# Kernel optimization log

Hardware: AMD Instinct MI355X
Metric: run time of the kernel (lower is better)

## Reference

```python
import jax, jax.numpy as jnp
import numpy as np

N_NODES = 50000
N_EDGES = 800000
IN_DIM, H1, H2, OUT_DIM = 128, 117, 42, 24


def _glorot(key, fan_in, fan_out):
    lim = (6.0 / (fan_in + fan_out)) ** 0.5
    return jax.random.uniform(key, (fan_in, fan_out), jnp.float32, -lim, lim)


def setup_inputs() -> dict:
    key = jax.random.key(0)
    ks = jax.random.split(key, 16)
    x = jax.random.normal(ks[0], (N_NODES, IN_DIM), jnp.float32)
    edge_index = jax.random.randint(ks[1], (2, N_EDGES), 0, N_NODES, dtype=jnp.int64)
    dims = [(IN_DIM, H1), (H1, H2), (H2, OUT_DIM), (H2, OUT_DIM)]
    names = ["1", "2", "mu", "lv"]
    inp = {"x": x, "edge_index": edge_index}
    for i, ((di, do), nm) in enumerate(zip(dims, names)):
        inp[f"Wl_{nm}"] = _glorot(ks[2 + 3 * i], di, do)      # weight on aggregated neighbors
        inp[f"Wr_{nm}"] = _glorot(ks[3 + 3 * i], di, do)      # root (self) weight
        inp[f"b_{nm}"] = jnp.zeros((do,), jnp.float32)
    return inp


def _sage_conv(x, src, dst, Wl, Wr, b):
    # mean-aggregate source features onto target nodes (PyG SAGEConv, aggr='mean')
    agg = jax.ops.segment_sum(x[src], dst, num_segments=N_NODES)      # [N, d_in]
    deg = jax.ops.segment_sum(jnp.ones((src.shape[0], 1), x.dtype), dst,
                              num_segments=N_NODES)                    # [N, 1]
    agg = agg / jnp.maximum(deg, 1.0)
    return agg @ Wl + x @ Wr + b


def reference(x, edge_index, Wl_1, Wr_1, b_1, Wl_2, Wr_2, b_2,
              Wl_mu, Wr_mu, b_mu, Wl_lv, Wr_lv, b_lv):
    src, dst = edge_index[0], edge_index[1]
    h = jax.nn.relu(_sage_conv(x, src, dst, Wl_1, Wr_1, b_1))          # dropout = identity (eval)
    h = jax.nn.relu(_sage_conv(h, src, dst, Wl_2, Wr_2, b_2))
    mu = _sage_conv(h, src, dst, Wl_mu, Wr_mu, b_mu)
    logvar = _sage_conv(h, src, dst, Wl_lv, Wr_lv, b_lv)
    return (mu, logvar)
```

## Files before the change

### kernel.cpp

```cpp
#include <hip/hip_runtime.h>

#define N_NODES 50000
#define N_EDGES 800000
#define CAP 64
#define ZROW 50000

typedef _Float16 f16;
typedef unsigned short u16;
typedef f16 f16x2 __attribute__((ext_vector_type(2)));
typedef f16 f16x4 __attribute__((ext_vector_type(4)));
typedef f16 f16x8 __attribute__((ext_vector_type(8)));
typedef float f32x4 __attribute__((ext_vector_type(4)));

#if __has_builtin(__builtin_amdgcn_fdot2)
#define FDOT2(a, b, c) __builtin_amdgcn_fdot2((a), (b), (c), false)
#else
#define FDOT2(a, b, c) ((c) + (float)(a).x * (float)(b).x + (float)(a).y * (float)(b).y)
#endif

__global__ void k_fill(u16* __restrict__ bucket, int* __restrict__ cnt,
                       f16* __restrict__ t1l, f16* __restrict__ t2l,
                       f16* __restrict__ p) {
    int gt = blockIdx.x * 256 + threadIdx.x;
    if (gt < 400000) {
        uint4 pat = {0xC350C350u, 0xC350C350u, 0xC350C350u, 0xC350C350u};
        ((uint4*)bucket)[gt] = pat;
    }
    if (gt < N_NODES) cnt[gt] = 0;
    if (blockIdx.x == 1599) {
        int t = threadIdx.x;
        if (t < 64)       ((unsigned*)t1l)[(size_t)ZROW * 64 + t] = 0u;
        else if (t < 96)  ((unsigned*)t2l)[(size_t)ZROW * 32 + (t - 64)] = 0u;
        else if (t < 128) ((unsigned*)p)[(size_t)ZROW * 32 + (t - 96)] = 0u;
    }
}

__global__ void k_build(const int* __restrict__ ei, int* __restrict__ cnt,
                        u16* __restrict__ bucket) {
    int e = blockIdx.x * blockDim.x + threadIdx.x;
    if (e >= N_EDGES) return;
    int s = ei[e];
    int d = ei[N_EDGES + e];
    int pos = atomicAdd(&cnt[d], 1);
    if (pos < CAP) bucket[d * CAP + pos] = (u16)s;
}

__global__ void k_packw(const float* __restrict__ Wl1, const float* __restrict__ Wr1,
                        const float* __restrict__ Wl2, const float* __restrict__ Wr2,
                        const float* __restrict__ Wlm, const float* __restrict__ Wrm,
                        const float* __restrict__ Wlv, const float* __restrict__ Wrv,
                        f16x2* __restrict__ w2p, f16* __restrict__ w1b,
                        f16* __restrict__ w2b) {
    int t = blockIdx.x * blockDim.x + threadIdx.x;
    if (t < 42 * 48) {
        int k = t / 48, j = t % 48;
        int o = (j < 24) ? j : j - 24;
        const float* L = (j < 24) ? Wlm : Wlv;
        const float* R = (j < 24) ? Wrm : Wrv;
        f16x2 w; w.x = (f16)L[k * 24 + o]; w.y = (f16)R[k * 24 + o];
        w2p[t] = w;
    }
    if (t < 15 * 4 * 64 * 8) {
        int f = t >> 9;
        int r = t & 511;
        int lane = r >> 3, j = r & 7;
        int nt = f >> 2, s = f & 3;
        int k = s * 32 + (lane >> 4) * 8 + j;
        int col = nt * 16 + (lane & 15);
        float v = 0.f;
        if (col < 117) v = Wl1[k * 117 + col];
        else if (col < 234) v = Wr1[k * 117 + (col - 117)];
        w1b[t] = (f16)v;
    }
    if (t < 6 * 4 * 64 * 8) {
        int f = t >> 9;
        int r = t & 511;
        int lane = r >> 3, j = r & 7;
        int nt = f >> 2, s = f & 3;
        int k = s * 32 + (lane >> 4) * 8 + j;
        int col = nt * 16 + (lane & 15);
        float v = 0.f;
        if (k < 117) {
            if (col < 42)      v = Wl2[k * 42 + col];
            else if (col < 84) v = Wr2[k * 42 + (col - 42)];
        }
        w2b[t] = (f16)v;
    }
}

__global__ __launch_bounds__(256) void k_gemm1(const float* __restrict__ x,
                        const f16* __restrict__ w1b, const float* __restrict__ b1,
                        f16* __restrict__ t1l, float* __restrict__ t1r) {
    int base = blockIdx.x * 16;
    int t = threadIdx.x;
    __shared__ __align__(16) f16 xa[16 * 128];
    {
        int row = t >> 4, kc = t & 15;
        const float4* xp = (const float4*)(x + (size_t)(base + row) * 128 + kc * 8);
        float4 x0 = xp[0], x1 = xp[1];
        f16x8 hv;
        hv[0] = (f16)x0.x; hv[1] = (f16)x0.y; hv[2] = (f16)x0.z; hv[3] = (f16)x0.w;
        hv[4] = (f16)x1.x; hv[5] = (f16)x1.y; hv[6] = (f16)x1.z; hv[7] = (f16)x1.w;
        int byte = row * 256 + ((kc ^ (row & 7)) << 4);
        *(f16x8*)((char*)xa + byte) = hv;
    }
    __syncthreads();
    int lane = t & 63, w = t >> 6;
    int hi = lane >> 4, lo = lane & 15;
    f16x8 a[4];
#pragma unroll
    for (int s = 0; s < 4; ++s) {
        int kchunk = s * 4 + hi;
        int byte = lo * 256 + ((kchunk ^ (lo & 7)) << 4);
        a[s] = *(const f16x8*)((const char*)xa + byte);
    }
    int ntiles = (w < 3) ? 4 : 3;
    for (int i = 0; i < ntiles; ++i) {
        int nt = w * 4 + i;
        const f16x8* bp = (const f16x8*)w1b + (size_t)(nt * 4) * 64 + lane;
        f32x4 acc = {0.f, 0.f, 0.f, 0.f};
#pragma unroll
        for (int s = 0; s < 4; ++s)
            acc = __builtin_amdgcn_mfma_f32_16x16x32_f16(a[s], bp[s * 64], acc, 0, 0, 0);
        int gcol = nt * 16 + lo;
#pragma unroll
        for (int r = 0; r < 4; ++r) {
            int grow = base + hi * 4 + r;
            float val = acc[r];
            if (gcol < 117) {
                t1l[(size_t)grow * 128 + gcol] = (f16)val;
            } else if (nt == 7) {
                t1l[(size_t)grow * 128 + gcol] = (f16)0.f;
            }
            if (gcol >= 117) {
                int c2 = gcol - 117;
                if (c2 < 117)      t1r[(size_t)grow * 120 + c2] = val + b1[c2];
                else if (c2 < 120) t1r[(size_t)grow * 120 + c2] = 0.f;
            }
        }
    }
}

__global__ __launch_bounds__(512) void k_fused1(
        const f16* __restrict__ t1l, const float* __restrict__ t1r,
        const int* __restrict__ cnt, const u16* __restrict__ bucket,
        const f16* __restrict__ w2b, const float* __restrict__ b2,
        f16* __restrict__ t2l, float* __restrict__ s2) {
    __shared__ __align__(16) f16 h1[16 * 128];
    int t = threadIdx.x;
    int lane = t & 63, w = t >> 6;
    int tilebase = blockIdx.x * 16;
    int iA = tilebase + w * 2, iB = iA + 1;
    int cA = cnt[iA], cB = cnt[iB];
    int nA = cA > CAP ? CAP : cA, nB = cB > CAP ? CAP : cB;
    int idsA = (int)bucket[(size_t)iA * CAP + lane];
    int idsB = (int)bucket[(size_t)iB * CAP + lane];
    int g = (lane < 30) ? 0 : 1;
    int d = lane - 30 * g;
    bool act = (lane < 60);
    int i_my = g ? iB : iA;
    float deg = fmaxf((float)(g ? cB : cA), 1.f);
    int dd = d < 31 ? d : 31;
    int nmax = nA > nB ? nA : nB;
    float ax = 0.f, ay = 0.f, az = 0.f, aw = 0.f;
    const char* base = (const char*)t1l;
    const f16x2 e10 = {(f16)1.f, (f16)0.f};
    const f16x2 e01 = {(f16)0.f, (f16)1.f};
    for (int e0 = 0; e0 < nmax; e0 += 16) {
        f16x4 v[16];
#pragma unroll
        for (int u = 0; u < 16; ++u) {
            int e = (e0 + u) & 63;
            int ra = __builtin_amdgcn_readlane(idsA, e);
            int rb = __builtin_amdgcn_readlane(idsB, e);
            int id = g ? rb : ra;
            unsigned off = ((unsigned)id << 8) + ((unsigned)dd << 3);
            v[u] = *(const f16x4*)(base + off);
        }
#pragma unroll
        for (int u = 0; u < 16; ++u) {
            f16x2 lo = __builtin_shufflevector(v[u], v[u], 0, 1);
            f16x2 hi2 = __builtin_shufflevector(v[u], v[u], 2, 3);
            ax = FDOT2(lo, e10, ax);
            ay = FDOT2(lo, e01, ay);
            az = FDOT2(hi2, e10, az);
            aw = FDOT2(hi2, e01, aw);
        }
    }
    int trow = w * 2 + g;
    if (act) {
        float4 s = ((const float4*)(t1r + (size_t)i_my * 120))[d];
        f16x4 hv;
        hv.x = (f16)fmaxf(ax / deg + s.x, 0.f);
        hv.y = (f16)fmaxf(ay / deg + s.y, 0.f);
        hv.z = (f16)fmaxf(az / deg + s.z, 0.f);
        hv.w = (f16)fmaxf(aw / deg + s.w, 0.f);
        int chunk = d >> 1;
        int byte = trow * 256 + ((chunk ^ (trow & 7)) << 4) + ((d & 1) << 3);
        *(f16x4*)((char*)h1 + byte) = hv;
    } else {
        int r2 = w * 2 + ((lane - 60) >> 1);
        int byte = r2 * 256 + ((15 ^ (r2 & 7)) << 4) + ((lane & 1) << 3);
        f16x4 z = {(f16)0.f, (f16)0.f, (f16)0.f, (f16)0.f};
        *(f16x4*)((char*)h1 + byte) = z;
    }
    __syncthreads();
    if (w < 6) {
        int lo = lane & 15, hi = lane >> 4;
        f16x8 a[4];
#pragma unroll
        for (int s = 0; s < 4; ++s) {
            int kc = s * 4 + hi;
            int byte = lo * 256 + ((kc ^ (lo & 7)) << 4);
            a[s] = *(const f16x8*)((const char*)h1 + byte);
        }
        const f16x8* bp = (const f16x8*)w2b + (size_t)(w * 4) * 64 + lane;
        f32x4 acc = {0.f, 0.f, 0.f, 0.f};
#pragma unroll
        for (int s = 0; s < 4; ++s)
            acc = __builtin_amdgcn_mfma_f32_16x16x32_f16(a[s], bp[s * 64], acc, 0, 0, 0);
        int col = w * 16 + lo;
        if (col < 42) {
#pragma unroll
            for (int r = 0; r < 4; ++r) {
                int node = tilebase + hi * 4 + r;
                t2l[(size_t)node * 64 + col] = (f16)acc[r];
            }
        } else if (col < 84) {
            int c2 = col - 42;
            float bb = b2[c2];
#pragma unroll
            for (int r = 0; r < 4; ++r) {
                int node = tilebase + hi * 4 + r;
                s2[(size_t)node * 42 + c2] = acc[r] + bb;
            }
        }
    }
}

__global__ __launch_bounds__(128) void k_fused2(
        const f16* __restrict__ t2l, const float* __restrict__ s2,
        const int* __restrict__ cnt, const u16* __restrict__ bucket,
        const f16x2* __restrict__ w2p,
        const float* __restrict__ bm, const float* __restrict__ bv,
        f16* __restrict__ p, float* __restrict__ out) {
    __shared__ __align__(16) float h2[2][3][48];
    int t = threadIdx.x;
    int lane = t & 63, wv = t >> 6;
    int i0 = blockIdx.x * 6 + wv * 3;
    int iA = i0, iB = i0 + 1, iC = i0 + 2;
    bool vA = iA < N_NODES, vB = iB < N_NODES, vC = iC < N_NODES;
    int cA = vA ? cnt[iA] : 0, cB = vB ? cnt[iB] : 0, cC = vC ? cnt[iC] : 0;
    int nA = cA > CAP ? CAP : cA, nB = cB > CAP ? CAP : cB, nC = cC > CAP ? CAP : cC;
    int idsA = vA ? (int)bucket[(size_t)iA * CAP + lane] : ZROW;
    int idsB = vB ? (int)bucket[(size_t)iB * CAP + lane] : ZROW;
    int idsC = vC ? (int)bucket[(size_t)iC * CAP + lane] : ZROW;
    int g = (lane < 21) ? 0 : (lane < 42 ? 1 : 2);
    int d = lane - 21 * g;
    bool act = (lane < 63);
    int i_my = i0 + g;
    bool valid = act && (i_my < N_NODES);
    float deg = fmaxf((float)(g == 0 ? cA : (g == 1 ? cB : cC)), 1.f);
    int nmax = nA > nB ? nA : nB; if (nC > nmax) nmax = nC;
    float ax = 0.f, ay = 0.f;
    const char* base = (const char*)t2l;
    const f16x2 e10 = {(f16)1.f, (f16)0.f};
    const f16x2 e01 = {(f16)0.f, (f16)1.f};
    for (int e0 = 0; e0 < nmax; e0 += 16) {
        f16x2 v[16];
#pragma unroll
        for (int u = 0; u < 16; ++u) {
            int e = (e0 + u) & 63;
            int ra = __builtin_amdgcn_readlane(idsA, e);
            int rb = __builtin_amdgcn_readlane(idsB, e);
            int rc = __builtin_amdgcn_readlane(idsC, e);
            int id = (g == 0) ? ra : ((g == 1) ? rb : rc);
            unsigned off = ((unsigned)id << 7) + ((unsigned)d << 2);
            v[u] = *(const f16x2*)(base + off);
        }
#pragma unroll
        for (int u = 0; u < 16; ++u) {
            ax = FDOT2(v[u], e10, ax);
            ay = FDOT2(v[u], e01, ay);
        }
    }
    if (valid && d < 21) {
        float2 s = ((const float2*)(s2 + (size_t)i_my * 42))[d];
        h2[wv][g][2 * d]     = fmaxf(ax / deg + s.x, 0.f);
        h2[wv][g][2 * d + 1] = fmaxf(ay / deg + s.y, 0.f);
    }
    __syncthreads();
    int j = lane;
    if (j < 48) {
        int o = (j < 24) ? j : j - 24;
        float bias = (j < 24) ? bm[o] : bv[o];
        float pA = 0.f, pB = 0.f, pC = 0.f, qA = 0.f, qB = 0.f, qC = 0.f;
        const float4* hA = (const float4*)&h2[wv][0][0];
        const float4* hB = (const float4*)&h2[wv][1][0];
        const float4* hC = (const float4*)&h2[wv][2][0];
#pragma unroll 2
        for (int kk = 0; kk < 10; ++kk) {
            float4 a = hA[kk], b = hB[kk], c = hC[kk];
            float av[4] = {a.x, a.y, a.z, a.w};
            float bv4[4] = {b.x, b.y, b.z, b.w};
            float cv[4] = {c.x, c.y, c.z, c.w};
#pragma unroll
            for (int u = 0; u < 4; ++u) {
                int k = 4 * kk + u;
                f16x2 wvv = w2p[k * 48 + j];
                float wl = (float)wvv.x, wr = (float)wvv.y;
                pA = fmaf(av[u], wl, pA);  qA = fmaf(av[u], wr, qA);
                pB = fmaf(bv4[u], wl, pB); qB = fmaf(bv4[u], wr, qB);
                pC = fmaf(cv[u], wl, pC);  qC = fmaf(cv[u], wr, qC);
            }
        }
        for (int k = 40; k < 42; ++k) {
            f16x2 wvv = w2p[k * 48 + j];
            float wl = (float)wvv.x, wr = (float)wvv.y;
            pA = fmaf(h2[wv][0][k], wl, pA); qA = fmaf(h2[wv][0][k], wr, qA);
            pB = fmaf(h2[wv][1][k], wl, pB); qB = fmaf(h2[wv][1][k], wr, qB);
            pC = fmaf(h2[wv][2][k], wl, pC); qC = fmaf(h2[wv][2][k], wr, qC);
        }
        size_t half = (j < 24) ? 0 : (size_t)N_NODES * 24;
        if (vA) { p[(size_t)iA * 64 + j] = (f16)pA; out[half + (size_t)iA * 24 + o] = qA + bias; }
        if (vB) { p[(size_t)iB * 64 + j] = (f16)pB; out[half + (size_t)iB * 24 + o] = qB + bias; }
        if (vC) { p[(size_t)iC * 64 + j] = (f16)pC; out[half + (size_t)iC * 24 + o] = qC + bias; }
    }
}

__global__ __launch_bounds__(128) void k_final(
        const f16* __restrict__ p, const int* __restrict__ cnt,
        const u16* __restrict__ bucket, float* __restrict__ out) {
    int t = threadIdx.x;
    int lane = t & 63, wv = t >> 6;
    int iA = blockIdx.x * 4 + wv * 2, iB = iA + 1;
    int cA = cnt[iA], cB = cnt[iB];
    int nA = cA > CAP ? CAP : cA, nB = cB > CAP ? CAP : cB;
    int idsA = (int)bucket[(size_t)iA * CAP + lane];
    int idsB = (int)bucket[(size_t)iB * CAP + lane];
    int g = (lane < 24) ? 0 : 1;
    int d = lane - 24 * g;
    bool act = (lane < 48);
    int i_my = g ? iB : iA;
    float deg = fmaxf((float)(g ? cB : cA), 1.f);
    int dd = d < 31 ? d : 31;
    int nmax = nA > nB ? nA : nB;
    float ax = 0.f, ay = 0.f;
    const char* base = (const char*)p;
    const f16x2 e10 = {(f16)1.f, (f16)0.f};
    const f16x2 e01 = {(f16)0.f, (f16)1.f};
    for (int e0 = 0; e0 < nmax; e0 += 16) {
        f16x2 v[16];
#pragma unroll
        for (int u = 0; u < 16; ++u) {
            int e = (e0 + u) & 63;
            int ra = __builtin_amdgcn_readlane(idsA, e);
            int rb = __builtin_amdgcn_readlane(idsB, e);
            int id = g ? rb : ra;
            unsigned off = ((unsigned)id << 7) + ((unsigned)dd << 2);
            v[u] = *(const f16x2*)(base + off);
        }
#pragma unroll
        for (int u = 0; u < 16; ++u) {
            ax = FDOT2(v[u], e10, ax);
            ay = FDOT2(v[u], e01, ay);
        }
    }
    if (act) {
        float mx = ax / deg, my = ay / deg;
        size_t addr = (d < 12) ? ((size_t)i_my * 24 + 2 * d)
                               : ((size_t)N_NODES * 24 + (size_t)i_my * 24 + 2 * (d - 12));
        float2 s = *(const float2*)(out + addr);
        float2 r; r.x = s.x + mx; r.y = s.y + my;
        *(float2*)(out + addr) = r;
    }
}

extern "C" void kernel_launch(void* const* d_in, const int* in_sizes, int n_in,
                              void* d_out, int out_size, void* d_ws, size_t ws_size,
                              hipStream_t stream) {
    const float* x   = (const float*)d_in[0];
    const int*   ei  = (const int*)d_in[1];
    const float* Wl1 = (const float*)d_in[2];
    const float* Wr1 = (const float*)d_in[3];
    const float* b1  = (const float*)d_in[4];
    const float* Wl2 = (const float*)d_in[5];
    const float* Wr2 = (const float*)d_in[6];
    const float* b2  = (const float*)d_in[7];
    const float* Wlm = (const float*)d_in[8];
    const float* Wrm = (const float*)d_in[9];
    const float* bm  = (const float*)d_in[10];
    const float* Wlv = (const float*)d_in[11];
    const float* Wrv = (const float*)d_in[12];
    const float* bv  = (const float*)d_in[13];
    float* out = (float*)d_out;

    char* ws = (char*)d_ws;
    int*   cnt    = (int*)(ws);
    u16*   bucket = (u16*)(ws + 204800);
    f16*   t1l    = (f16*)(ws + 6604800);
    float* t1r    = (float*)(ws + 19405312);
    f16*   t2l    = (f16*)(ws + 43405312);
    float* s2     = (float*)(ws + 49805824);
    f16*   w1b    = (f16*)(ws + 49805824);
    f16*   p      = (f16*)(ws + 58205824);
    f16x2* w2p    = (f16x2*)(ws + 64606208);
    f16*   w2b    = (f16*)(ws + 64614400);

    k_fill<<<1600, 256, 0, stream>>>(bucket, cnt, t1l, t2l, p);
    k_packw<<<120, 256, 0, stream>>>(Wl1, Wr1, Wl2, Wr2, Wlm, Wrm, Wlv, Wrv,
                                     w2p, w1b, w2b);
    k_build<<<(N_EDGES + 255) / 256, 256, 0, stream>>>(ei, cnt, bucket);
    k_gemm1<<<N_NODES / 16, 256, 0, stream>>>(x, w1b, b1, t1l, t1r);
    k_fused1<<<N_NODES / 16, 512, 0, stream>>>(t1l, t1r, cnt, bucket, w2b, b2, t2l, s2);
    k_fused2<<<(N_NODES + 5) / 6, 128, 0, stream>>>(t2l, s2, cnt, bucket,
                                                    w2p, bm, bv, p, out);
    k_final<<<N_NODES / 4, 128, 0, stream>>>(p, cnt, bucket, out);
}
```

Baseline: 247.5 us.

## Merge setup kernels, stage neighbor ids in LDS, use 16-byte gathers and MFMA heads

After: 209.4 us. -15.4%, faster.

```diff
diff --git a/kernel.cpp b/kernel.cpp
--- a/kernel.cpp
+++ b/kernel.cpp
@@ -18,9 +18,15 @@
 #define FDOT2(a, b, c) ((c) + (float)(a).x * (float)(b).x + (float)(a).y * (float)(b).y)
 #endif
 
-__global__ void k_fill(u16* __restrict__ bucket, int* __restrict__ cnt,
-                       f16* __restrict__ t1l, f16* __restrict__ t2l,
-                       f16* __restrict__ p) {
+__global__ void k_fillpack(u16* __restrict__ bucket, int* __restrict__ cnt,
+                           f16* __restrict__ t1l, f16* __restrict__ t2l,
+                           f16* __restrict__ p,
+                           const float* __restrict__ Wl1, const float* __restrict__ Wr1,
+                           const float* __restrict__ Wl2, const float* __restrict__ Wr2,
+                           const float* __restrict__ Wlm, const float* __restrict__ Wrm,
+                           const float* __restrict__ Wlv, const float* __restrict__ Wrv,
+                           f16* __restrict__ w1b, f16* __restrict__ w2b,
+                           f16* __restrict__ w3b) {
     int gt = blockIdx.x * 256 + threadIdx.x;
     if (gt < 400000) {
         uint4 pat = {0xC350C350u, 0xC350C350u, 0xC350C350u, 0xC350C350u};
@@ -33,36 +39,8 @@
         else if (t < 96)  ((unsigned*)t2l)[(size_t)ZROW * 32 + (t - 64)] = 0u;
         else if (t < 128) ((unsigned*)p)[(size_t)ZROW * 32 + (t - 96)] = 0u;
     }
-}
-
-__global__ void k_build(const int* __restrict__ ei, int* __restrict__ cnt,
-                        u16* __restrict__ bucket) {
-    int e = blockIdx.x * blockDim.x + threadIdx.x;
-    if (e >= N_EDGES) return;
-    int s = ei[e];
-    int d = ei[N_EDGES + e];
-    int pos = atomicAdd(&cnt[d], 1);
-    if (pos < CAP) bucket[d * CAP + pos] = (u16)s;
-}
-
-__global__ void k_packw(const float* __restrict__ Wl1, const float* __restrict__ Wr1,
-                        const float* __restrict__ Wl2, const float* __restrict__ Wr2,
-                        const float* __restrict__ Wlm, const float* __restrict__ Wrm,
-                        const float* __restrict__ Wlv, const float* __restrict__ Wrv,
-                        f16x2* __restrict__ w2p, f16* __restrict__ w1b,
-                        f16* __restrict__ w2b) {
-    int t = blockIdx.x * blockDim.x + threadIdx.x;
-    if (t < 42 * 48) {
-        int k = t / 48, j = t % 48;
-        int o = (j < 24) ? j : j - 24;
-        const float* L = (j < 24) ? Wlm : Wlv;
-        const float* R = (j < 24) ? Wrm : Wrv;
-        f16x2 w; w.x = (f16)L[k * 24 + o]; w.y = (f16)R[k * 24 + o];
-        w2p[t] = w;
-    }
-    if (t < 15 * 4 * 64 * 8) {
-        int f = t >> 9;
-        int r = t & 511;
+    if (gt < 15 * 4 * 64 * 8) {
+        int f = gt >> 9, r = gt & 511;
         int lane = r >> 3, j = r & 7;
         int nt = f >> 2, s = f & 3;
         int k = s * 32 + (lane >> 4) * 8 + j;
@@ -70,29 +48,50 @@
         float v = 0.f;
         if (col < 117) v = Wl1[k * 117 + col];
         else if (col < 234) v = Wr1[k * 117 + (col - 117)];
-        w1b[t] = (f16)v;
-    }
-    if (t < 6 * 4 * 64 * 8) {
-        int f = t >> 9;
-        int r = t & 511;
+        w1b[gt] = (f16)v;
+    }
+    if (gt < 6 * 4 * 64 * 8) {
+        int f = gt >> 9, r = gt & 511;
         int lane = r >> 3, j = r & 7;
         int nt = f >> 2, s = f & 3;
         int k = s * 32 + (lane >> 4) * 8 + j;
         int col = nt * 16 + (lane & 15);
         float v = 0.f;
         if (k < 117) {
-            if (col < 42)      v = Wl2[k * 42 + col];
-            else if (col < 84) v = Wr2[k * 42 + (col - 42)];
-        }
-        w2b[t] = (f16)v;
-    }
-}
-
-__global__ __launch_bounds__(256) void k_gemm1(const float* __restrict__ x,
+            if (col < 42)                     v = Wl2[k * 42 + col];
+            else if (col >= 48 && col < 90)   v = Wr2[k * 42 + (col - 48)];
+        }
+        w2b[gt] = (f16)v;
+    }
+    if (gt < 6 * 2 * 64 * 8) {
+        int f = gt >> 9, r = gt & 511;
+        int lane = r >> 3, j = r & 7;
+        int ct = f >> 1, s = f & 1;
+        int k = s * 32 + (lane >> 4) * 8 + j;
+        int col = ct * 16 + (lane & 15);
+        float v = 0.f;
+        if (k < 42) {
+            if (col < 24)      v = Wlm[k * 24 + col];
+            else if (col < 48) v = Wlv[k * 24 + (col - 24)];
+            else if (col < 72) v = Wrm[k * 24 + (col - 48)];
+            else               v = Wrv[k * 24 + (col - 72)];
+        }
+        w3b[gt] = (f16)v;
+    }
+}
+
+__global__ __launch_bounds__(256) void k_bg(const int* __restrict__ ei,
+                        int* __restrict__ cnt, u16* __restrict__ bucket,
+                        const float* __restrict__ x,
                         const f16* __restrict__ w1b, const float* __restrict__ b1,
                         f16* __restrict__ t1l, float* __restrict__ t1r) {
+    int t = threadIdx.x;
+    int e = blockIdx.x * 256 + t;
+    int se = ei[e];
+    int de = ei[N_EDGES + e];
+    int pos = atomicAdd(&cnt[de], 1);
+
     int base = blockIdx.x * 16;
-    int t = threadIdx.x;
     __shared__ __align__(16) f16 xa[16 * 128];
     {
         int row = t >> 4, kc = t & 15;
@@ -139,6 +138,7 @@
             }
         }
     }
+    if (pos < CAP) bucket[de * CAP + pos] = (u16)se;
 }
 
 __global__ __launch_bounds__(512) void k_fused1(
@@ -146,93 +146,89 @@
         const int* __restrict__ cnt, const u16* __restrict__ bucket,
         const f16* __restrict__ w2b, const float* __restrict__ b2,
         f16* __restrict__ t2l, float* __restrict__ s2) {
-    __shared__ __align__(16) f16 h1[16 * 128];
+    __shared__ __align__(16) f16 h1[32 * 128];
+    __shared__ __align__(16) u16 ids[32 * 72];
     int t = threadIdx.x;
     int lane = t & 63, w = t >> 6;
-    int tilebase = blockIdx.x * 16;
-    int iA = tilebase + w * 2, iB = iA + 1;
-    int cA = cnt[iA], cB = cnt[iB];
-    int nA = cA > CAP ? CAP : cA, nB = cB > CAP ? CAP : cB;
-    int idsA = (int)bucket[(size_t)iA * CAP + lane];
-    int idsB = (int)bucket[(size_t)iB * CAP + lane];
-    int g = (lane < 30) ? 0 : 1;
-    int d = lane - 30 * g;
-    bool act = (lane < 60);
-    int i_my = g ? iB : iA;
-    float deg = fmaxf((float)(g ? cB : cA), 1.f);
-    int dd = d < 31 ? d : 31;
-    int nmax = nA > nB ? nA : nB;
-    float ax = 0.f, ay = 0.f, az = 0.f, aw = 0.f;
-    const char* base = (const char*)t1l;
+    int tilebase = blockIdx.x * 32;
+    if (t < 256) {
+        uint4 q = ((const uint4*)(bucket + (size_t)tilebase * CAP))[t];
+        int nl = t >> 3, c = t & 7;
+        *(uint4*)(ids + nl * 72 + c * 8) = q;
+    }
+    int g = (lane < 60) ? (lane / 15) : 3;
+    int d = (lane < 60) ? (lane - g * 15) : 14;
+    int nl = w * 4 + g;
+    int i_my = tilebase + nl;
+    int c = (i_my < N_NODES && lane < 60) ? cnt[i_my] : 0;
+    int n = min(c, CAP);
+    float deg = fmaxf((float)c, 1.f);
+    int n0 = __builtin_amdgcn_readlane(n, 0),  n1 = __builtin_amdgcn_readlane(n, 15);
+    int n2 = __builtin_amdgcn_readlane(n, 30), n3 = __builtin_amdgcn_readlane(n, 45);
+    int nmax = max(max(n0, n1), max(n2, n3));
+    __syncthreads();
+    float acc[8] = {0.f, 0.f, 0.f, 0.f, 0.f, 0.f, 0.f, 0.f};
+    const char* tb = (const char*)t1l;
+    unsigned doff = (unsigned)d * 16;
     const f16x2 e10 = {(f16)1.f, (f16)0.f};
     const f16x2 e01 = {(f16)0.f, (f16)1.f};
-    for (int e0 = 0; e0 < nmax; e0 += 16) {
-        f16x4 v[16];
-#pragma unroll
-        for (int u = 0; u < 16; ++u) {
-            int e = (e0 + u) & 63;
-            int ra = __builtin_amdgcn_readlane(idsA, e);
-            int rb = __builtin_amdgcn_readlane(idsB, e);
-            int id = g ? rb : ra;
-            unsigned off = ((unsigned)id << 8) + ((unsigned)dd << 3);
-            v[u] = *(const f16x4*)(base + off);
-        }
-#pragma unroll
-        for (int u = 0; u < 16; ++u) {
-            f16x2 lo = __builtin_shufflevector(v[u], v[u], 0, 1);
-            f16x2 hi2 = __builtin_shufflevector(v[u], v[u], 2, 3);
-            ax = FDOT2(lo, e10, ax);
-            ay = FDOT2(lo, e01, ay);
-            az = FDOT2(hi2, e10, az);
-            aw = FDOT2(hi2, e01, aw);
-        }
-    }
-    int trow = w * 2 + g;
-    if (act) {
-        float4 s = ((const float4*)(t1r + (size_t)i_my * 120))[d];
-        f16x4 hv;
-        hv.x = (f16)fmaxf(ax / deg + s.x, 0.f);
-        hv.y = (f16)fmaxf(ay / deg + s.y, 0.f);
-        hv.z = (f16)fmaxf(az / deg + s.z, 0.f);
-        hv.w = (f16)fmaxf(aw / deg + s.w, 0.f);
-        int chunk = d >> 1;
-        int byte = trow * 256 + ((chunk ^ (trow & 7)) << 4) + ((d & 1) << 3);
-        *(f16x4*)((char*)h1 + byte) = hv;
+    int idb = nl * 72;
+    for (int e0 = 0; e0 < nmax; e0 += 8) {
+        f16x8 v[8];
+#pragma unroll
+        for (int u = 0; u < 8; ++u) {
+            unsigned id = ids[idb + e0 + u];
+            v[u] = *(const f16x8*)(tb + id * 256u + doff);
+        }
+#pragma unroll
+        for (int u = 0; u < 8; ++u) {
+            const f16x2* pv = (const f16x2*)&v[u];
+#pragma unroll
+            for (int j = 0; j < 4; ++j) {
+                acc[2 * j]     = FDOT2(pv[j], e10, acc[2 * j]);
+                acc[2 * j + 1] = FDOT2(pv[j], e01, acc[2 * j + 1]);
+            }
+        }
+    }
+    if (lane < 60) {
+        int i_ld = (i_my < N_NODES) ? i_my : 0;
+        const float4* sp = (const float4*)(t1r + (size_t)i_ld * 120 + 8 * d);
+        float4 s0 = sp[0], s1 = sp[1];
+        float sv[8] = {s0.x, s0.y, s0.z, s0.w, s1.x, s1.y, s1.z, s1.w};
+        f16x8 hv;
+#pragma unroll
+        for (int j = 0; j < 8; ++j) hv[j] = (f16)fmaxf(acc[j] / deg + sv[j], 0.f);
+        int byte = nl * 256 + ((d ^ (nl & 7)) << 4);
+        *(f16x8*)((char*)h1 + byte) = hv;
     } else {
-        int r2 = w * 2 + ((lane - 60) >> 1);
-        int byte = r2 * 256 + ((15 ^ (r2 & 7)) << 4) + ((lane & 1) << 3);
-        f16x4 z = {(f16)0.f, (f16)0.f, (f16)0.f, (f16)0.f};
-        *(f16x4*)((char*)h1 + byte) = z;
-    }
-    __syncthreads();
-    if (w < 6) {
-        int lo = lane & 15, hi = lane >> 4;
+        int row = w * 4 + (lane - 60);
+        int byte = row * 256 + ((15 ^ (row & 7)) << 4);
+        f16x8 z = {};
+        *(f16x8*)((char*)h1 + byte) = z;
+    }
+    __syncthreads();
+    int lo = lane & 15, hi = lane >> 4;
+    for (int jj = w; jj < 12; jj += 8) {
+        int ct = jj >> 1, rh = jj & 1;
+        int row = rh * 16 + lo;
         f16x8 a[4];
 #pragma unroll
         for (int s = 0; s < 4; ++s) {
             int kc = s * 4 + hi;
-            int byte = lo * 256 + ((kc ^ (lo & 7)) << 4);
-            a[s] = *(const f16x8*)((const char*)h1 + byte);
-        }
-        const f16x8* bp = (const f16x8*)w2b + (size_t)(w * 4) * 64 + lane;
-        f32x4 acc = {0.f, 0.f, 0.f, 0.f};
+            a[s] = *(const f16x8*)((const char*)h1 + row * 256 + ((kc ^ (row & 7)) << 4));
+        }
+        const f16x8* bp = (const f16x8*)w2b + (size_t)(ct * 4) * 64 + lane;
+        f32x4 acc4 = {0.f, 0.f, 0.f, 0.f};
 #pragma unroll
         for (int s = 0; s < 4; ++s)
-            acc = __builtin_amdgcn_mfma_f32_16x16x32_f16(a[s], bp[s * 64], acc, 0, 0, 0);
-        int col = w * 16 + lo;
-        if (col < 42) {
-#pragma unroll
-            for (int r = 0; r < 4; ++r) {
-                int node = tilebase + hi * 4 + r;
-                t2l[(size_t)node * 64 + col] = (f16)acc[r];
-            }
-        } else if (col < 84) {
-            int c2 = col - 42;
-            float bb = b2[c2];
-#pragma unroll
-            for (int r = 0; r < 4; ++r) {
-                int node = tilebase + hi * 4 + r;
-                s2[(size_t)node * 42 + c2] = acc[r] + bb;
+            acc4 = __builtin_amdgcn_mfma_f32_16x16x32_f16(a[s], bp[s * 64], acc4, 0, 0, 0);
+        int col = ct * 16 + lo;
+#pragma unroll
+        for (int r = 0; r < 4; ++r) {
+            int node = tilebase + rh * 16 + hi * 4 + r;
+            if (node < N_NODES) {
+                if (col < 48)      t2l[(size_t)node * 64 + col] = (f16)acc4[r];
+                else if (col < 90) s2[(size_t)node * 42 + (col - 48)] = acc4[r] + b2[col - 48];
             }
         }
     }
@@ -241,138 +237,166 @@
 __global__ __launch_bounds__(128) void k_fused2(
         const f16* __restrict__ t2l, const float* __restrict__ s2,
         const int* __restrict__ cnt, const u16* __restrict__ bucket,
-        const f16x2* __restrict__ w2p,
+        const f16* __restrict__ w3b,
         const float* __restrict__ bm, const float* __restrict__ bv,
         f16* __restrict__ p, float* __restrict__ out) {
-    __shared__ __align__(16) float h2[2][3][48];
+    __shared__ __align__(16) f16 h2[16 * 64];
+    __shared__ __align__(16) u16 ids[16 * 72];
     int t = threadIdx.x;
     int lane = t & 63, wv = t >> 6;
-    int i0 = blockIdx.x * 6 + wv * 3;
-    int iA = i0, iB = i0 + 1, iC = i0 + 2;
-    bool vA = iA < N_NODES, vB = iB < N_NODES, vC = iC < N_NODES;
-    int cA = vA ? cnt[iA] : 0, cB = vB ? cnt[iB] : 0, cC = vC ? cnt[iC] : 0;
-    int nA = cA > CAP ? CAP : cA, nB = cB > CAP ? CAP : cB, nC = cC > CAP ? CAP : cC;
-    int idsA = vA ? (int)bucket[(size_t)iA * CAP + lane] : ZROW;
-    int idsB = vB ? (int)bucket[(size_t)iB * CAP + lane] : ZROW;
-    int idsC = vC ? (int)bucket[(size_t)iC * CAP + lane] : ZROW;
-    int g = (lane < 21) ? 0 : (lane < 42 ? 1 : 2);
-    int d = lane - 21 * g;
-    bool act = (lane < 63);
-    int i_my = i0 + g;
-    bool valid = act && (i_my < N_NODES);
-    float deg = fmaxf((float)(g == 0 ? cA : (g == 1 ? cB : cC)), 1.f);
-    int nmax = nA > nB ? nA : nB; if (nC > nmax) nmax = nC;
-    float ax = 0.f, ay = 0.f;
-    const char* base = (const char*)t2l;
+    int nb = blockIdx.x * 16;
+    {
+        uint4 q = ((const uint4*)(bucket + (size_t)nb * CAP))[t];
+        int nl = t >> 3, c = t & 7;
+        *(uint4*)(ids + nl * 72 + c * 8) = q;
+    }
+    int g = (lane < 48) ? (lane / 6) : 7;
+    int d = (lane < 48) ? (lane - g * 6) : 5;
+    int nl = wv * 8 + g;
+    int i_my = nb + nl;
+    int c = (lane < 48) ? cnt[i_my] : 0;
+    int n = min(c, CAP);
+    float deg = fmaxf((float)c, 1.f);
+    int nmax = n;
+#pragma unroll
+    for (int m = 1; m < 64; m <<= 1) nmax = max(nmax, __shfl_xor(nmax, m));
+    __syncthreads();
+    float acc[8] = {0.f, 0.f, 0.f, 0.f, 0.f, 0.f, 0.f, 0.f};
+    const char* tb = (const char*)t2l;
+    unsigned doff = (unsigned)d * 16;
     const f16x2 e10 = {(f16)1.f, (f16)0.f};
     const f16x2 e01 = {(f16)0.f, (f16)1.f};
-    for (int e0 = 0; e0 < nmax; e0 += 16) {
-        f16x2 v[16];
-#pragma unroll
-        for (int u = 0; u < 16; ++u) {
-            int e = (e0 + u) & 63;
-            int ra = __builtin_amdgcn_readlane(idsA, e);
-            int rb = __builtin_amdgcn_readlane(idsB, e);
-            int rc = __builtin_amdgcn_readlane(idsC, e);
-            int id = (g == 0) ? ra : ((g == 1) ? rb : rc);
-            unsigned off = ((unsigned)id << 7) + ((unsigned)d << 2);
-            v[u] = *(const f16x2*)(base + off);
-        }
-#pragma unroll
-        for (int u = 0; u < 16; ++u) {
-            ax = FDOT2(v[u], e10, ax);
-            ay = FDOT2(v[u], e01, ay);
-        }
-    }
-    if (valid && d < 21) {
-        float2 s = ((const float2*)(s2 + (size_t)i_my * 42))[d];
-        h2[wv][g][2 * d]     = fmaxf(ax / deg + s.x, 0.f);
-        h2[wv][g][2 * d + 1] = fmaxf(ay / deg + s.y, 0.f);
-    }
-    __syncthreads();
-    int j = lane;
-    if (j < 48) {
-        int o = (j < 24) ? j : j - 24;
-        float bias = (j < 24) ? bm[o] : bv[o];
-        float pA = 0.f, pB = 0.f, pC = 0.f, qA = 0.f, qB = 0.f, qC = 0.f;
-        const float4* hA = (const float4*)&h2[wv][0][0];
-        const float4* hB = (const float4*)&h2[wv][1][0];
-        const float4* hC = (const float4*)&h2[wv][2][0];
-#pragma unroll 2
-        for (int kk = 0; kk < 10; ++kk) {
-            float4 a = hA[kk], b = hB[kk], c = hC[kk];
-            float av[4] = {a.x, a.y, a.z, a.w};
-            float bv4[4] = {b.x, b.y, b.z, b.w};
-            float cv[4] = {c.x, c.y, c.z, c.w};
-#pragma unroll
-            for (int u = 0; u < 4; ++u) {
-                int k = 4 * kk + u;
-                f16x2 wvv = w2p[k * 48 + j];
-                float wl = (float)wvv.x, wr = (float)wvv.y;
-                pA = fmaf(av[u], wl, pA);  qA = fmaf(av[u], wr, qA);
-                pB = fmaf(bv4[u], wl, pB); qB = fmaf(bv4[u], wr, qB);
-                pC = fmaf(cv[u], wl, pC);  qC = fmaf(cv[u], wr, qC);
-            }
-        }
-        for (int k = 40; k < 42; ++k) {
-            f16x2 wvv = w2p[k * 48 + j];
-            float wl = (float)wvv.x, wr = (float)wvv.y;
-            pA = fmaf(h2[wv][0][k], wl, pA); qA = fmaf(h2[wv][0][k], wr, qA);
-            pB = fmaf(h2[wv][1][k], wl, pB); qB = fmaf(h2[wv][1][k], wr, qB);
-            pC = fmaf(h2[wv][2][k], wl, pC); qC = fmaf(h2[wv][2][k], wr, qC);
-        }
-        size_t half = (j < 24) ? 0 : (size_t)N_NODES * 24;
-        if (vA) { p[(size_t)iA * 64 + j] = (f16)pA; out[half + (size_t)iA * 24 + o] = qA + bias; }
-        if (vB) { p[(size_t)iB * 64 + j] = (f16)pB; out[half + (size_t)iB * 24 + o] = qB + bias; }
-        if (vC) { p[(size_t)iC * 64 + j] = (f16)pC; out[half + (size_t)iC * 24 + o] = qC + bias; }
+    int idb = nl * 72;
+    for (int e0 = 0; e0 < nmax; e0 += 8) {
+        f16x8 v[8];
+#pragma unroll
+        for (int u = 0; u < 8; ++u) {
+            unsigned id = ids[idb + e0 + u];
+            v[u] = *(const f16x8*)(tb + id * 128u + doff);
+        }
+#pragma unroll
+        for (int u = 0; u < 8; ++u) {
+            const f16x2* pv = (const f16x2*)&v[u];
+#pragma unroll
+            for (int j = 0; j < 4; ++j) {
+                acc[2 * j]     = FDOT2(pv[j], e10, acc[2 * j]);
+                acc[2 * j + 1] = FDOT2(pv[j], e01, acc[2 * j + 1]);
+            }
+        }
+    }
+    if (lane < 48) {
+        float sv[8];
+        if (d < 5) {
+            const float4* sp = (const float4*)(s2 + (size_t)i_my * 42 + 8 * d);
+            float4 s0 = sp[0], s1 = sp[1];
+            sv[0] = s0.x; sv[1] = s0.y; sv[2] = s0.z; sv[3] = s0.w;
+            sv[4] = s1.x; sv[5] = s1.y; sv[6] = s1.z; sv[7] = s1.w;
+        } else {
+            float2 s0 = *(const float2*)(s2 + (size_t)i_my * 42 + 40);
+            sv[0] = s0.x; sv[1] = s0.y;
+            sv[2] = sv[3] = sv[4] = sv[5] = sv[6] = sv[7] = 0.f;
+        }
+        f16x8 hv;
+#pragma unroll
+        for (int j = 0; j < 8; ++j) hv[j] = (f16)fmaxf(acc[j] / deg + sv[j], 0.f);
+        int byte = nl * 128 + ((d ^ (nl & 7)) << 4);
+        *(f16x8*)((char*)h2 + byte) = hv;
+    } else {
+        int j = lane - 48;
+        int row = wv * 8 + (j >> 1);
+        int chunk = 6 + (j & 1);
+        int byte = row * 128 + ((chunk ^ (row & 7)) << 4);
+        f16x8 z = {};
+        *(f16x8*)((char*)h2 + byte) = z;
+    }
+    __syncthreads();
+    int lo = lane & 15, hi = lane >> 4;
+    f16x8 a2[2];
+#pragma unroll
+    for (int s = 0; s < 2; ++s) {
+        int kc = s * 4 + hi;
+        a2[s] = *(const f16x8*)((const char*)h2 + lo * 128 + ((kc ^ (lo & 7)) << 4));
+    }
+#pragma unroll
+    for (int i = 0; i < 3; ++i) {
+        int ct = wv * 3 + i;
+        const f16x8* bp = (const f16x8*)w3b + (size_t)(ct * 2) * 64 + lane;
+        f32x4 acc4 = {0.f, 0.f, 0.f, 0.f};
+        acc4 = __builtin_amdgcn_mfma_f32_16x16x32_f16(a2[0], bp[0], acc4, 0, 0, 0);
+        acc4 = __builtin_amdgcn_mfma_f32_16x16x32_f16(a2[1], bp[64], acc4, 0, 0, 0);
+        int col = ct * 16 + lo;
+#pragma unroll
+        for (int r = 0; r < 4; ++r) {
+            int node = nb + hi * 4 + r;
+            if (col < 48) {
+                p[(size_t)node * 64 + col] = (f16)acc4[r];
+            } else {
+                int o = col - 48;
+                if (o < 24) out[(size_t)node * 24 + o] = acc4[r] + bm[o];
+                else out[(size_t)N_NODES * 24 + (size_t)node * 24 + (o - 24)] = acc4[r] + bv[o - 24];
+            }
+        }
     }
 }
 
 __global__ __launch_bounds__(128) void k_final(
         const f16* __restrict__ p, const int* __restrict__ cnt,
         const u16* __restrict__ bucket, float* __restrict__ out) {
+    __shared__ __align__(16) u16 ids[20 * 72];
     int t = threadIdx.x;
     int lane = t & 63, wv = t >> 6;
-    int iA = blockIdx.x * 4 + wv * 2, iB = iA + 1;
-    int cA = cnt[iA], cB = cnt[iB];
-    int nA = cA > CAP ? CAP : cA, nB = cB > CAP ? CAP : cB;
-    int idsA = (int)bucket[(size_t)iA * CAP + lane];
-    int idsB = (int)bucket[(size_t)iB * CAP + lane];
-    int g = (lane < 24) ? 0 : 1;
-    int d = lane - 24 * g;
-    bool act = (lane < 48);
-    int i_my = g ? iB : iA;
-    float deg = fmaxf((float)(g ? cB : cA), 1.f);
-    int dd = d < 31 ? d : 31;
-    int nmax = nA > nB ? nA : nB;
-    float ax = 0.f, ay = 0.f;
-    const char* base = (const char*)p;
+    int nb = blockIdx.x * 20;
+    for (int s = t; s < 160; s += 128) {
+        uint4 q = ((const uint4*)(bucket + (size_t)nb * CAP))[s];
+        int nl = s >> 3, c = s & 7;
+        *(uint4*)(ids + nl * 72 + c * 8) = q;
+    }
+    int g = (lane < 60) ? (lane / 6) : 9;
+    int d = (lane < 60) ? (lane - g * 6) : 5;
+    int nl = wv * 10 + g;
+    int i_my = nb + nl;
+    int c = (lane < 60) ? cnt[i_my] : 0;
+    int n = min(c, CAP);
+    float deg = fmaxf((float)c, 1.f);
+    int nmax = n;
+#pragma unroll
+    for (int m = 1; m < 64; m <<= 1) nmax = max(nmax, __shfl_xor(nmax, m));
+    __syncthreads();
+    float acc[8] = {0.f, 0.f, 0.f, 0.f, 0.f, 0.f, 0.f, 0.f};
+    const char* pb = (const char*)p;
+    unsigned doff = (unsigned)d * 16;
     const f16x2 e10 = {(f16)1.f, (f16)0.f};
     const f16x2 e01 = {(f16)0.f, (f16)1.f};
-    for (int e0 = 0; e0 < nmax; e0 += 16) {
-        f16x2 v[16];
-#pragma unroll
-        for (int u = 0; u < 16; ++u) {
-            int e = (e0 + u) & 63;
-            int ra = __builtin_amdgcn_readlane(idsA, e);
-            int rb = __builtin_amdgcn_readlane(idsB, e);
-            int id = g ? rb : ra;
-            unsigned off = ((unsigned)id << 7) + ((unsigned)dd << 2);
-            v[u] = *(const f16x2*)(base + off);
-        }
-#pragma unroll
-        for (int u = 0; u < 16; ++u) {
-            ax = FDOT2(v[u], e10, ax);
-            ay = FDOT2(v[u], e01, ay);
-        }
-    }
-    if (act) {
-        float mx = ax / deg, my = ay / deg;
-        size_t addr = (d < 12) ? ((size_t)i_my * 24 + 2 * d)
-                               : ((size_t)N_NODES * 24 + (size_t)i_my * 24 + 2 * (d - 12));
-        float2 s = *(const float2*)(out + addr);
-        float2 r; r.x = s.x + mx; r.y = s.y + my;
-        *(float2*)(out + addr) = r;
+    int idb = nl * 72;
+    for (int e0 = 0; e0 < nmax; e0 += 8) {
+        f16x8 v[8];
+#pragma unroll
+        for (int u = 0; u < 8; ++u) {
+            unsigned id = ids[idb + e0 + u];
+            v[u] = *(const f16x8*)(pb + id * 128u + doff);
+        }
+#pragma unroll
+        for (int u = 0; u < 8; ++u) {
+            const f16x2* pv = (const f16x2*)&v[u];
+#pragma unroll
+            for (int j = 0; j < 4; ++j) {
+                acc[2 * j]     = FDOT2(pv[j], e10, acc[2 * j]);
+                acc[2 * j + 1] = FDOT2(pv[j], e01, acc[2 * j + 1]);
+            }
+        }
+    }
+    if (lane < 60) {
+        float rdeg = 1.f / deg;
+        size_t base = (d < 3) ? ((size_t)i_my * 24 + 8 * d)
+                              : ((size_t)N_NODES * 24 + (size_t)i_my * 24 + 8 * (d - 3));
+        float4 o0 = *(const float4*)(out + base);
+        float4 o1 = *(const float4*)(out + base + 4);
+        o0.x += acc[0] * rdeg; o0.y += acc[1] * rdeg;
+        o0.z += acc[2] * rdeg; o0.w += acc[3] * rdeg;
+        o1.x += acc[4] * rdeg; o1.y += acc[5] * rdeg;
+        o1.z += acc[6] * rdeg; o1.w += acc[7] * rdeg;
+        *(float4*)(out + base) = o0;
+        *(float4*)(out + base + 4) = o1;
     }
 }
 
@@ -404,16 +428,14 @@
     float* s2     = (float*)(ws + 49805824);
     f16*   w1b    = (f16*)(ws + 49805824);
     f16*   p      = (f16*)(ws + 58205824);
-    f16x2* w2p    = (f16x2*)(ws + 64606208);
-    f16*   w2b    = (f16*)(ws + 64614400);
-
-    k_fill<<<1600, 256, 0, stream>>>(bucket, cnt, t1l, t2l, p);
-    k_packw<<<120, 256, 0, stream>>>(Wl1, Wr1, Wl2, Wr2, Wlm, Wrm, Wlv, Wrv,
-                                     w2p, w1b, w2b);
-    k_build<<<(N_EDGES + 255) / 256, 256, 0, stream>>>(ei, cnt, bucket);
-    k_gemm1<<<N_NODES / 16, 256, 0, stream>>>(x, w1b, b1, t1l, t1r);
-    k_fused1<<<N_NODES / 16, 512, 0, stream>>>(t1l, t1r, cnt, bucket, w2b, b2, t2l, s2);
-    k_fused2<<<(N_NODES + 5) / 6, 128, 0, stream>>>(t2l, s2, cnt, bucket,
-                                                    w2p, bm, bv, p, out);
-    k_final<<<N_NODES / 4, 128, 0, stream>>>(p, cnt, bucket, out);
-}
+    f16*   w2b    = (f16*)(ws + 64606208);
+    f16*   w3b    = (f16*)(ws + 64630784);
+
+    k_fillpack<<<1600, 256, 0, stream>>>(bucket, cnt, t1l, t2l, p,
+                                         Wl1, Wr1, Wl2, Wr2, Wlm, Wrm, Wlv, Wrv,
+                                         w1b, w2b, w3b);
+    k_bg<<<3125, 256, 0, stream>>>(ei, cnt, bucket, x, w1b, b1, t1l, t1r);
+    k_fused1<<<1563, 512, 0, stream>>>(t1l, t1r, cnt, bucket, w2b, b2, t2l, s2);
+    k_fused2<<<3125, 128, 0, stream>>>(t2l, s2, cnt, bucket, w3b, bm, bv, p, out);
+    k_final<<<2500, 128, 0, stream>>>(p, cnt, bucket, out);
+}
```
